# Performance work log

Measured on AMD Instinct MI355X. Metric: run time of the kernel, lower is better.

The kernel has to match this reference:

```python
import jax, jax.numpy as jnp
import numpy as np
import math

B, S, D = 1, 1024, 4096
H, HD, KVH = 32, 128, 8
R, FF = 16, 14336
EPS = 1e-5


def setup_inputs() -> dict:
    key = jax.random.key(0)
    ks = jax.random.split(key, 32)
    def nrm(i, shape, scale):
        return jax.random.normal(ks[i], shape, dtype=jnp.float32) * scale
    inp = {}
    inp["x"] = nrm(0, (B, S, D), 0.5)
    inp["norm_w1"] = jnp.ones((D,), jnp.float32)
    inp["norm_w2"] = jnp.ones((D,), jnp.float32)
    # rotary embedding tables (Mistral theta=10000)
    inv_freq = 1.0 / (10000.0 ** (jnp.arange(0, HD, 2, dtype=jnp.float32) / HD))
    freqs = jnp.outer(jnp.arange(S, dtype=jnp.float32), inv_freq)
    emb = jnp.concatenate([freqs, freqs], axis=-1)  # [S, HD]
    inp["cos"] = jnp.cos(emb)
    inp["sin"] = jnp.sin(emb)
    causal = jnp.tril(jnp.ones((S, S), dtype=bool))
    inp["mask"] = jnp.where(causal, 0.0, -1e9).astype(jnp.float32)[None, None]  # [1,1,S,S]
    w_shapes = {"wq": (D, D), "wk": (KVH * HD, D), "wv": (KVH * HD, D),
                "wo": (D, D), "wg": (FF, D), "wu": (FF, D), "wd": (D, FF)}
    i = 1
    for name, shp in w_shapes.items():
        inp[name] = nrm(i, shp, 0.02); i += 1
        dout, din = shp
        inp["la_" + name[1]] = nrm(i, (din, R), 0.02); i += 1
        inp["lb_" + name[1]] = nrm(i, (R, dout), 0.02); i += 1
    inp["num_heads"] = H
    inp["head_dim"] = HD
    inp["num_kv_heads"] = KVH
    return inp


def _rms(x, w):
    # rmsnorm_forward with eps=1e-5, weight only
    return x * jax.lax.rsqrt(jnp.mean(x * x, axis=-1, keepdims=True) + EPS) * w


def _lora(x, W, la, lb):
    # dequantized base weight [out,in] applied as x @ W.T, plus low-rank delta
    return x @ W.T + (x @ la) @ lb


def _rope(x, cos, sin):
    # x: [B, h, S, HD]; rotate_half convention
    x1, x2 = jnp.split(x, 2, axis=-1)
    rot = jnp.concatenate([-x2, x1], axis=-1)
    return x * cos[None, None] + rot * sin[None, None]


def _layer(x, norm_w1, norm_w2, cos, sin, mask,
           wq, la_q, lb_q, wk, la_k, lb_k, wv, la_v, lb_v, wo, la_o, lb_o,
           wg, la_g, lb_g, wu, la_u, lb_u, wd, la_d, lb_d,
           num_heads, head_dim, num_kv_heads):
    b, s, d = x.shape
    n_rep = num_heads // num_kv_heads
    xn1 = _rms(x, norm_w1)
    q = _lora(xn1, wq, la_q, lb_q).reshape(b, s, num_heads, head_dim).transpose(0, 2, 1, 3)
    k = _lora(xn1, wk, la_k, lb_k).reshape(b, s, num_kv_heads, head_dim).transpose(0, 2, 1, 3)
    v = _lora(xn1, wv, la_v, lb_v).reshape(b, s, num_kv_heads, head_dim).transpose(0, 2, 1, 3)
    q = _rope(q, cos, sin)
    k = _rope(k, cos, sin)
    k = jnp.repeat(k, n_rep, axis=1)
    v = jnp.repeat(v, n_rep, axis=1)
    scores = jnp.einsum("bhqd,bhkd->bhqk", q, k) / math.sqrt(head_dim) + mask
    a = jax.nn.softmax(scores, axis=-1)
    o = jnp.einsum("bhqk,bhkd->bhqd", a, v).transpose(0, 2, 1, 3).reshape(b, s, d)
    o = _lora(o, wo, la_o, lb_o)
    x_med = x + o
    xn2 = _rms(x_med, norm_w2)
    gate = _lora(xn2, wg, la_g, lb_g)
    up = _lora(xn2, wu, la_u, lb_u)
    h = jax.nn.silu(gate) * up
    down = _lora(h, wd, la_d, lb_d)
    return x_med + down


def reference(x, norm_w1, norm_w2, cos, sin, mask,
              wq, la_q, lb_q, wk, la_k, lb_k, wv, la_v, lb_v, wo, la_o, lb_o,
              wg, la_g, lb_g, wu, la_u, lb_u, wd, la_d, lb_d,
              num_heads, head_dim, num_kv_heads):
    return _layer(x, norm_w1, norm_w2, cos, sin, mask,
                  wq, la_q, lb_q, wk, la_k, lb_k, wv, la_v, lb_v, wo, la_o, lb_o,
                  wg, la_g, lb_g, wu, la_u, lb_u, wd, la_d, lb_d,
                  num_heads, head_dim, num_kv_heads)
```

## Files before the change

### kernel.cpp

```cpp
#include <hip/hip_runtime.h>
#include <hip/hip_bf16.h>
#include <math.h>

#define SEQ 1024
#define DIM 4096
#define NH 32
#define HD 128
#define NKVH 8
#define FF 14336
#define LR 16

typedef __attribute__((ext_vector_type(8))) short bf16x8;
typedef __attribute__((ext_vector_type(4))) float f32x4;
typedef __attribute__((ext_vector_type(4))) ushort ushort4v;
typedef __attribute__((ext_vector_type(4))) unsigned int u32x4;

__device__ __forceinline__ ushort f2bf(float f) {
  union { float f; unsigned u; } v; v.f = f;
  unsigned r = (v.u + 0x7FFFu + ((v.u >> 16) & 1u)) >> 16;
  return (ushort)r;
}
__device__ __forceinline__ float bf2f(ushort h) {
  union { unsigned u; float f; } v; v.u = ((unsigned)h) << 16;
  return v.f;
}
__device__ __forceinline__ unsigned cvtpk(float a, float b) {
  unsigned r;
  asm("v_cvt_pk_bf16_f32 %0, %1, %2" : "=v"(r) : "v"(a), "v"(b));
  return r;
}

__device__ __forceinline__ void gload_lds16(const void* g, void* l) {
  __builtin_amdgcn_global_load_lds(
      (const __attribute__((address_space(1))) void*)g,
      (__attribute__((address_space(3))) void*)l, 16, 0, 0);
}

__global__ __launch_bounds__(256) void rmsnorm_kernel(const float* __restrict__ x,
                                                      const float* __restrict__ w,
                                                      ushort* __restrict__ out) {
  int row = blockIdx.x;
  int tid = threadIdx.x;
  const float* xr = x + (size_t)row * DIM;
  float vals[16];
  float s = 0.f;
#pragma unroll
  for (int c = 0; c < 4; c++) {
    float4 v = *(const float4*)&xr[(tid + c * 256) * 4];
    vals[c * 4 + 0] = v.x; vals[c * 4 + 1] = v.y;
    vals[c * 4 + 2] = v.z; vals[c * 4 + 3] = v.w;
    s += v.x * v.x + v.y * v.y + v.z * v.z + v.w * v.w;
  }
#pragma unroll
  for (int off = 32; off >= 1; off >>= 1) s += __shfl_down(s, off);
  __shared__ float wsum[4];
  __shared__ float scale_s;
  int lane = tid & 63, wv = tid >> 6;
  if (lane == 0) wsum[wv] = s;
  __syncthreads();
  if (tid == 0) {
    float t = wsum[0] + wsum[1] + wsum[2] + wsum[3];
    scale_s = rsqrtf(t / (float)DIM + 1e-5f);
  }
  __syncthreads();
  float scale = scale_s;
  ushort* orow = out + (size_t)row * DIM;
#pragma unroll
  for (int c = 0; c < 4; c++) {
    int base = (tid + c * 256) * 4;
    float4 wv4 = *(const float4*)&w[base];
    ushort4v ov;
    ov.x = f2bf(vals[c * 4 + 0] * scale * wv4.x);
    ov.y = f2bf(vals[c * 4 + 1] * scale * wv4.y);
    ov.z = f2bf(vals[c * 4 + 2] * scale * wv4.z);
    ov.w = f2bf(vals[c * 4 + 3] * scale * wv4.w);
    *(ushort4v*)&orow[base] = ov;
  }
}

template <int NL>
__global__ __launch_bounds__(256) void lora_a_kernel(
    const ushort* __restrict__ A,
    const float* __restrict__ la0, const float* __restrict__ la1,
    const float* __restrict__ la2,
    ushort* __restrict__ t0, ushort* __restrict__ t1, ushort* __restrict__ t2,
    int K) {
  int m = blockIdx.x, i = threadIdx.x;
  float acc[NL][16];
#pragma unroll
  for (int l = 0; l < NL; l++)
#pragma unroll
    for (int n = 0; n < 16; n++) acc[l][n] = 0.f;

  const ushort* Arow = A + (size_t)m * K;
  int nc = K >> 8;
  for (int c = 0; c < nc; c++) {
    int k = c * 256 + i;
    float a = bf2f(Arow[k]);
#pragma unroll
    for (int l = 0; l < NL; l++) {
      const float* lap = (l == 0 ? la0 : (l == 1 ? la1 : la2)) + (size_t)k * 16;
#pragma unroll
      for (int q = 0; q < 4; q++) {
        float4 lv = *(const float4*)&lap[q * 4];
        acc[l][q * 4 + 0] += a * lv.x;
        acc[l][q * 4 + 1] += a * lv.y;
        acc[l][q * 4 + 2] += a * lv.z;
        acc[l][q * 4 + 3] += a * lv.w;
      }
    }
  }

  __shared__ float red[256][17];
  __shared__ float red2[16][17];
#pragma unroll
  for (int l = 0; l < NL; l++) {
    __syncthreads();
#pragma unroll
    for (int n = 0; n < 16; n++) red[i][n] = acc[l][n];
    __syncthreads();
    {
      int g = i >> 4, n = i & 15;
      float s = 0.f;
#pragma unroll
      for (int j = 0; j < 16; j++) s += red[g * 16 + j][n];
      red2[g][n] = s;
    }
    __syncthreads();
    if (i < 16) {
      float s2 = 0.f;
#pragma unroll
      for (int g2 = 0; g2 < 16; g2++) s2 += red2[g2][i];
      ushort* tp = (l == 0 ? t0 : (l == 1 ? t1 : t2));
      tp[(size_t)m * LR + i] = f2bf(s2);
    }
  }
}

template <int WM>
__global__ __launch_bounds__(512) void gemm256_kernel(
    const ushort* __restrict__ A,
    const float* __restrict__ W0, const float* __restrict__ W1, const float* __restrict__ W2,
    const float* __restrict__ lb0, const float* __restrict__ lb1, const float* __restrict__ lb2,
    const ushort* __restrict__ t0, const ushort* __restrict__ t1, const ushort* __restrict__ t2,
    void* __restrict__ o0, void* __restrict__ o1, void* __restrict__ o2,
    int c1, int c2, void* __restrict__ outp, int M, int N, int K, int nkp) {
  __shared__ __align__(16) ushort As[2][256 * 64];
  __shared__ __align__(16) ushort Bs[2][256 * 64];
  int tid = threadIdx.x;
  int lane = tid & 63, wave = tid >> 6;
  int wm = wave >> 2, wn = wave & 3;

  int gx = gridDim.x, gy = gridDim.y, gz = gridDim.z;
  int flat = blockIdx.x + gx * (blockIdx.y + gy * blockIdx.z);
  int nwg = gx * gy * gz;
  int q = nwg >> 3, r = nwg & 7;
  int xcd = flat & 7;
  int wgid = (xcd < r ? xcd * (q + 1) : r * (q + 1) + (xcd - r) * q) + (flat >> 3);
  int sh = gy * gz;
  int bx = wgid / sh;
  int rem = wgid - bx * sh;
  int z = rem / gy;
  int by = rem - z * gy;

  int n0 = bx * 256, m0 = by * 256;
  int k0 = z * nkp;

  const float* Wp; const float* lbp; const ushort* tp; void* osel; int nseg, wseg;
  if (n0 < c1)      { Wp = W0; lbp = lb0; tp = t0; osel = o0; nseg = n0;      wseg = c1; }
  else if (n0 < c2) { Wp = W1; lbp = lb1; tp = t1; osel = o1; nseg = n0 - c1; wseg = c2 - c1; }
  else              { Wp = W2; lbp = lb2; tp = t2; osel = o2; nseg = n0 - c2; wseg = N - c2; }

  int srow = tid >> 3;
  int sswz = ((tid & 7) ^ (srow & 7)) * 8;
  const ushort* Ab = A + (size_t)(m0 + srow) * K + sswz;
  const float* Wbase = Wp + (size_t)(nseg + srow) * K + (tid & 7) * 8;

  f32x4 acc[8][4] = {};
  float4 breg[8];

#define SHALF(kt, b, h)                                                       \
  _Pragma("unroll") for (int i = 2 * (h); i < 2 * (h) + 2; i++) {             \
    gload_lds16(Ab + (size_t)(i * 64) * K + (size_t)(kt) * 64,                \
                &As[b][wave * 512 + i * 4096]);                               \
  }
#define BLOAD(kt, h)                                                          \
  {                                                                           \
    const float* gp = Wbase + (size_t)((h) * 128) * K + (size_t)(kt) * 64;    \
    breg[(h) * 4 + 0] = *(const float4*)gp;                                   \
    breg[(h) * 4 + 1] = *(const float4*)(gp + 4);                             \
    breg[(h) * 4 + 2] = *(const float4*)(gp + (size_t)64 * K);                \
    breg[(h) * 4 + 3] = *(const float4*)(gp + (size_t)64 * K + 4);            \
  }
#define WRITE_B(b)                                                            \
  _Pragma("unroll") for (int h = 0; h < 2; h++)                               \
  _Pragma("unroll") for (int j = 0; j < 2; j++) {                             \
    int rr = h * 128 + j * 64 + srow;                                         \
    float4 lo = breg[h * 4 + j * 2 + 0];                                      \
    float4 hi = breg[h * 4 + j * 2 + 1];                                      \
    u32x4 v;                                                                  \
    v.x = cvtpk(lo.x, lo.y); v.y = cvtpk(lo.z, lo.w);                         \
    v.z = cvtpk(hi.x, hi.y); v.w = cvtpk(hi.z, hi.w);                         \
    *(u32x4*)&Bs[b][rr * 64 + (((tid & 7) ^ (rr & 7))) * 8] = v;              \
  }
#define LDFRAG(buf, rr, ks) \
  (*(const bf16x8*)&(buf)[(rr) * 64 + (((ks) * 4 + (lane >> 4)) ^ ((rr) & 7)) * 8])

  BLOAD(k0, 0); BLOAD(k0, 1);
  SHALF(k0, 0, 0); SHALF(k0, 0, 1);
  asm volatile("s_waitcnt vmcnt(4)" ::: "memory");
  WRITE_B(0);
  if (nkp > 1) { BLOAD(k0 + 1, 0); BLOAD(k0 + 1, 1); }
  if (nkp > 1) asm volatile("s_waitcnt vmcnt(8)" ::: "memory");
  else         asm volatile("s_waitcnt vmcnt(0)" ::: "memory");
  asm volatile("s_waitcnt lgkmcnt(0)" ::: "memory");
  __builtin_amdgcn_s_barrier();
  __builtin_amdgcn_sched_barrier(0);

  for (int tau = 0; tau < nkp; tau++) {
    int b = tau & 1;
    bool s1 = (tau + 1 < nkp), s2 = (tau + 2 < nkp);
    const ushort* as = As[b];
    const ushort* bs = Bs[b];
    bf16x8 bfr[4][2];
#pragma unroll
    for (int p = 0; p < 4; p++) {
      bf16x8 af[2][2];
#pragma unroll
      for (int qq = 0; qq < 2; qq++) {
        int ra = wm * 128 + (p * 2 + qq) * 16 + (lane & 15);
#pragma unroll
        for (int ks = 0; ks < 2; ks++) af[qq][ks] = LDFRAG(as, ra, ks);
      }
      if (p == 0) {
#pragma unroll
        for (int f = 0; f < 4; f++) {
          int rb = wn * 64 + f * 16 + (lane & 15);
#pragma unroll
          for (int ks = 0; ks < 2; ks++) bfr[f][ks] = LDFRAG(bs, rb, ks);
        }
      }
      if (p == 0 && s1) { SHALF(k0 + tau + 1, b ^ 1, 0); }
      if (p == 1 && s1) { SHALF(k0 + tau + 1, b ^ 1, 1); }
      if (p == 2 && s2) { BLOAD(k0 + tau + 2, 0); }
      if (p == 3 && s2) { BLOAD(k0 + tau + 2, 1); }
      __builtin_amdgcn_sched_barrier(0);
      __builtin_amdgcn_s_barrier();
      asm volatile("s_waitcnt lgkmcnt(0)" ::: "memory");
      __builtin_amdgcn_sched_barrier(0);
      __builtin_amdgcn_s_setprio(1);
#pragma unroll
      for (int qq = 0; qq < 2; qq++)
#pragma unroll
        for (int fn = 0; fn < 4; fn++)
#pragma unroll
          for (int ks = 0; ks < 2; ks++)
            acc[p * 2 + qq][fn] = __builtin_amdgcn_mfma_f32_16x16x32_bf16(
                af[qq][ks], bfr[fn][ks], acc[p * 2 + qq][fn], 0, 0, 0);
      __builtin_amdgcn_s_setprio(0);
      __builtin_amdgcn_sched_barrier(0);
      if (p == 1 && s1) {
        asm volatile("s_waitcnt vmcnt(4)" ::: "memory");
        WRITE_B(b ^ 1);
        __builtin_amdgcn_sched_barrier(0);
      }
      if (p == 3) {
        if (s2) asm volatile("s_waitcnt vmcnt(8)" ::: "memory");
        else    asm volatile("s_waitcnt vmcnt(0)" ::: "memory");
      }
      __builtin_amdgcn_s_barrier();
      __builtin_amdgcn_sched_barrier(0);
    }
  }
#undef SHALF
#undef BLOAD
#undef WRITE_B

  if (z == 0) {
#pragma unroll
    for (int it = 0; it < 2; it++) {
      int task = tid + it * 512;
      int rr = task >> 2, ls = task & 3;
      int ph = ls ^ (rr & 7);
      bf16x8 avv = {};
      bf16x8 bvv = {};
      if (ls < 2) {
        avv = *(const bf16x8*)&tp[(size_t)(m0 + rr) * LR + ls * 8];
#pragma unroll
        for (int j = 0; j < 8; j++)
          bvv[j] = (short)f2bf(lbp[(size_t)(ls * 8 + j) * wseg + nseg + rr]);
      }
      *(bf16x8*)&As[0][rr * 64 + ph * 8] = avv;
      *(bf16x8*)&Bs[0][rr * 64 + ph * 8] = bvv;
    }
    __syncthreads();
    bf16x8 af[8], bfr[4];
#pragma unroll
    for (int f = 0; f < 8; f++) {
      int ra = wm * 128 + f * 16 + (lane & 15);
      af[f] = LDFRAG(As[0], ra, 0);
    }
#pragma unroll
    for (int f = 0; f < 4; f++) {
      int rb = wn * 64 + f * 16 + (lane & 15);
      bfr[f] = LDFRAG(Bs[0], rb, 0);
    }
#pragma unroll
    for (int fm = 0; fm < 8; fm++)
#pragma unroll
      for (int fn = 0; fn < 4; fn++)
        acc[fm][fn] = __builtin_amdgcn_mfma_f32_16x16x32_bf16(af[fm], bfr[fn], acc[fm][fn], 0, 0, 0);
  }
#undef LDFRAG

#pragma unroll
  for (int fm = 0; fm < 8; fm++) {
#pragma unroll
    for (int j = 0; j < 4; j++) {
      int mg = m0 + wm * 128 + fm * 16 + (lane >> 4) * 4 + j;
#pragma unroll
      for (int fn = 0; fn < 4; fn++) {
        int ncol = wn * 64 + fn * 16 + (lane & 15);
        float v = acc[fm][fn][j];
        if (WM == 0) {
          ((ushort*)osel)[(size_t)mg * wseg + nseg + ncol] = f2bf(v);
        } else {
          ((float*)outp)[((size_t)z * M + mg) * (size_t)N + n0 + ncol] = v;
        }
      }
    }
  }
}

__global__ __launch_bounds__(256) void silu_mul_kernel(const ushort* __restrict__ g,
                                                       const ushort* __restrict__ u,
                                                       ushort* __restrict__ h) {
  size_t idx = (size_t)(blockIdx.x * 256 + threadIdx.x) * 8;
  bf16x8 gv = *(const bf16x8*)&g[idx];
  bf16x8 uv = *(const bf16x8*)&u[idx];
  bf16x8 hv;
#pragma unroll
  for (int i = 0; i < 8; i++) {
    float gf = bf2f((ushort)gv[i]);
    float uf = bf2f((ushort)uv[i]);
    float sv = gf / (1.f + __expf(-gf));
    hv[i] = (short)f2bf(sv * uf);
  }
  *(bf16x8*)&h[idx] = hv;
}

__global__ __launch_bounds__(256) void reduce2_qkv_rope(const float* __restrict__ p,
                                                        const float* __restrict__ ct,
                                                        const float* __restrict__ st,
                                                        ushort* __restrict__ qb,
                                                        ushort* __restrict__ kb,
                                                        ushort* __restrict__ vtb) {
  int gidx = blockIdx.x * 256 + threadIdx.x;
  int r = gidx / 896, j = gidx - r * 896;
  size_t row = (size_t)r * 6144;
  size_t sstride = (size_t)SEQ * 6144;
  if (j < 640) {
    bool isq = j < 512;
    int jj = isq ? j : j - 512;
    int h = jj >> 4, d0 = (jj & 15) * 4;
    size_t base = row + (isq ? 0 : DIM) + h * 128 + d0;
    float4 a1 = *(const float4*)&p[base];
    float4 b1 = *(const float4*)&p[base + sstride];
    float4 a2 = *(const float4*)&p[base + 64];
    float4 b2 = *(const float4*)&p[base + 64 + sstride];
    float4 x1, x2;
    x1.x = a1.x + b1.x; x1.y = a1.y + b1.y; x1.z = a1.z + b1.z; x1.w = a1.w + b1.w;
    x2.x = a2.x + b2.x; x2.y = a2.y + b2.y; x2.z = a2.z + b2.z; x2.w = a2.w + b2.w;
    float4 c = *(const float4*)&ct[r * HD + d0];
    float4 s = *(const float4*)&st[r * HD + d0];
    float sc = isq ? 0.08838834764831845f : 1.0f;
    ushort4v o1, o2;
    o1.x = f2bf((x1.x * c.x - x2.x * s.x) * sc);
    o1.y = f2bf((x1.y * c.y - x2.y * s.y) * sc);
    o1.z = f2bf((x1.z * c.z - x2.z * s.z) * sc);
    o1.w = f2bf((x1.w * c.w - x2.w * s.w) * sc);
    o2.x = f2bf((x2.x * c.x + x1.x * s.x) * sc);
    o2.y = f2bf((x2.y * c.y + x1.y * s.y) * sc);
    o2.z = f2bf((x2.z * c.z + x1.z * s.z) * sc);
    o2.w = f2bf((x2.w * c.w + x1.w * s.w) * sc);
    if (isq) {
      *(ushort4v*)&qb[(size_t)r * DIM + h * 128 + d0] = o1;
      *(ushort4v*)&qb[(size_t)r * DIM + h * 128 + d0 + 64] = o2;
    } else {
      *(ushort4v*)&kb[(size_t)r * 1024 + h * 128 + d0] = o1;
      *(ushort4v*)&kb[(size_t)r * 1024 + h * 128 + d0 + 64] = o2;
    }
  } else {
    int jj = j - 640;
    int c0 = jj * 4;
    size_t base = row + DIM + 1024 + c0;
    float4 a = *(const float4*)&p[base];
    float4 b = *(const float4*)&p[base + sstride];
    vtb[(size_t)(c0 + 0) * SEQ + r] = f2bf(a.x + b.x);
    vtb[(size_t)(c0 + 1) * SEQ + r] = f2bf(a.y + b.y);
    vtb[(size_t)(c0 + 2) * SEQ + r] = f2bf(a.z + b.z);
    vtb[(size_t)(c0 + 3) * SEQ + r] = f2bf(a.w + b.w);
  }
}

__global__ __launch_bounds__(256) void reduce4_res_kernel(const float* __restrict__ p,
                                                          const float* __restrict__ res,
                                                          float* __restrict__ out,
                                                          size_t sstride) {
  size_t i = ((size_t)blockIdx.x * 256 + threadIdx.x) * 4;
  float4 a = *(const float4*)&p[i];
  float4 b = *(const float4*)&p[i + sstride];
  float4 c = *(const float4*)&p[i + 2 * sstride];
  float4 d = *(const float4*)&p[i + 3 * sstride];
  float4 r = *(const float4*)&res[i];
  float4 o;
  o.x = a.x + b.x + c.x + d.x + r.x;
  o.y = a.y + b.y + c.y + d.y + r.y;
  o.z = a.z + b.z + c.z + d.z + r.z;
  o.w = a.w + b.w + c.w + d.w + r.w;
  *(float4*)&out[i] = o;
}

__global__ __launch_bounds__(256) void reduce4_res_rms(const float* __restrict__ p,
                                                       const float* __restrict__ res,
                                                       const float* __restrict__ w,
                                                       float* __restrict__ xmed,
                                                       ushort* __restrict__ xn2,
                                                       size_t sstride) {
  int row = blockIdx.x, tid = threadIdx.x;
  size_t base = (size_t)row * DIM;
  float vals[16];
  float sq = 0.f;
#pragma unroll
  for (int c = 0; c < 4; c++) {
    size_t i = base + (tid + c * 256) * 4;
    float4 a = *(const float4*)&p[i];
    float4 b = *(const float4*)&p[i + sstride];
    float4 cc = *(const float4*)&p[i + 2 * sstride];
    float4 d = *(const float4*)&p[i + 3 * sstride];
    float4 r = *(const float4*)&res[i];
    float4 v;
    v.x = a.x + b.x + cc.x + d.x + r.x;
    v.y = a.y + b.y + cc.y + d.y + r.y;
    v.z = a.z + b.z + cc.z + d.z + r.z;
    v.w = a.w + b.w + cc.w + d.w + r.w;
    *(float4*)&xmed[i] = v;
    vals[c * 4 + 0] = v.x; vals[c * 4 + 1] = v.y;
    vals[c * 4 + 2] = v.z; vals[c * 4 + 3] = v.w;
    sq += v.x * v.x + v.y * v.y + v.z * v.z + v.w * v.w;
  }
#pragma unroll
  for (int off = 32; off >= 1; off >>= 1) sq += __shfl_down(sq, off);
  __shared__ float wsum[4];
  __shared__ float scale_s;
  int lane = tid & 63, wv = tid >> 6;
  if (lane == 0) wsum[wv] = sq;
  __syncthreads();
  if (tid == 0) {
    float t = wsum[0] + wsum[1] + wsum[2] + wsum[3];
    scale_s = rsqrtf(t / (float)DIM + 1e-5f);
  }
  __syncthreads();
  float scale = scale_s;
#pragma unroll
  for (int c = 0; c < 4; c++) {
    int off = (tid + c * 256) * 4;
    float4 wv4 = *(const float4*)&w[off];
    ushort4v ov;
    ov.x = f2bf(vals[c * 4 + 0] * scale * wv4.x);
    ov.y = f2bf(vals[c * 4 + 1] * scale * wv4.y);
    ov.z = f2bf(vals[c * 4 + 2] * scale * wv4.z);
    ov.w = f2bf(vals[c * 4 + 3] * scale * wv4.w);
    *(ushort4v*)&xn2[base + off] = ov;
  }
}

__global__ __launch_bounds__(256) void attn_kernel(const ushort* __restrict__ q,
                                                   const ushort* __restrict__ k,
                                                   const ushort* __restrict__ vt,
                                                   ushort* __restrict__ o) {
  int flat = blockIdx.x + 16 * blockIdx.y;
  int kvh = flat & 7;
  int idx = flat >> 3;
  int h = kvh * 4 + (idx & 3);
  int qb = 15 - (idx >> 2);
  int tid = threadIdx.x, lane = tid & 63, wave = tid >> 6;
  __shared__ ushort Ks[64][136];
  __shared__ ushort Vs[128][72];
  __shared__ ushort Ps[4][16][72];

  bf16x8 qf[4];
  int qrow = qb * 64 + wave * 16 + (lane & 15);
#pragma unroll
  for (int kk = 0; kk < 4; kk++)
    qf[kk] = *(const bf16x8*)&q[(size_t)qrow * DIM + h * HD + kk * 32 + (lane >> 4) * 8];

  f32x4 oacc[8] = {};
  float mrow[4], lrow[4];
  int qr[4];
#pragma unroll
  for (int j = 0; j < 4; j++) {
    mrow[j] = -INFINITY; lrow[j] = 0.f;
    qr[j] = qb * 64 + wave * 16 + (lane >> 4) * 4 + j;
  }

  for (int kt = 0; kt <= qb; kt++) {
    int key0 = kt * 64;
#pragma unroll
    for (int c = 0; c < 4; c++) {
      int e = tid * 32 + c * 8;
      int r = e >> 7, cc = e & 127;
      *(bf16x8*)&Ks[r][cc] =
          *(const bf16x8*)&k[(size_t)(key0 + r) * (NKVH * HD) + kvh * HD + cc];
      int r2 = e >> 6, cc2 = e & 63;
      *(bf16x8*)&Vs[r2][cc2] =
          *(const bf16x8*)&vt[(size_t)(kvh * HD + r2) * SEQ + key0 + cc2];
    }
    __syncthreads();

    f32x4 sf[4] = {};
#pragma unroll
    for (int fn = 0; fn < 4; fn++)
#pragma unroll
      for (int kk = 0; kk < 4; kk++) {
        bf16x8 kf = *(const bf16x8*)&Ks[fn * 16 + (lane & 15)][kk * 32 + (lane >> 4) * 8];
        sf[fn] = __builtin_amdgcn_mfma_f32_16x16x32_bf16(qf[kk], kf, sf[fn], 0, 0, 0);
      }

#pragma unroll
    for (int fn = 0; fn < 4; fn++) {
      int key = key0 + fn * 16 + (lane & 15);
#pragma unroll
      for (int j = 0; j < 4; j++)
        if (key > qr[j]) sf[fn][j] = -INFINITY;
    }

#pragma unroll
    for (int j = 0; j < 4; j++) {
      float mx = fmaxf(fmaxf(sf[0][j], sf[1][j]), fmaxf(sf[2][j], sf[3][j]));
#pragma unroll
      for (int off = 1; off < 16; off <<= 1) mx = fmaxf(mx, __shfl_xor(mx, off));
      float mnew = fmaxf(mrow[j], mx);
      float sc = __expf(mrow[j] - mnew);
      mrow[j] = mnew;
      float rs = 0.f;
#pragma unroll
      for (int fn = 0; fn < 4; fn++) {
        float p = __expf(sf[fn][j] - mnew);
        sf[fn][j] = p;
        rs += p;
      }
#pragma unroll
      for (int off = 1; off < 16; off <<= 1) rs += __shfl_xor(rs, off);
      lrow[j] = lrow[j] * sc + rs;
#pragma unroll
      for (int f2 = 0; f2 < 8; f2++) oacc[f2][j] *= sc;
    }

#pragma unroll
    for (int fn = 0; fn < 4; fn++)
#pragma unroll
      for (int j = 0; j < 4; j++)
        Ps[wave][(lane >> 4) * 4 + j][fn * 16 + (lane & 15)] = f2bf(sf[fn][j]);

#pragma unroll
    for (int kk = 0; kk < 2; kk++) {
      bf16x8 pf = *(const bf16x8*)&Ps[wave][lane & 15][kk * 32 + (lane >> 4) * 8];
#pragma unroll
      for (int f2 = 0; f2 < 8; f2++) {
        bf16x8 vf = *(const bf16x8*)&Vs[f2 * 16 + (lane & 15)][kk * 32 + (lane >> 4) * 8];
        oacc[f2] = __builtin_amdgcn_mfma_f32_16x16x32_bf16(pf, vf, oacc[f2], 0, 0, 0);
      }
    }
    __syncthreads();
  }

#pragma unroll
  for (int j = 0; j < 4; j++) {
    float inv = 1.f / lrow[j];
#pragma unroll
    for (int f2 = 0; f2 < 8; f2++)
      o[(size_t)qr[j] * DIM + h * HD + f2 * 16 + (lane & 15)] = f2bf(oacc[f2][j] * inv);
  }
}

extern "C" void kernel_launch(void* const* d_in, const int* in_sizes, int n_in,
                              void* d_out, int out_size, void* d_ws, size_t ws_size,
                              hipStream_t stream) {
  const float* x    = (const float*)d_in[0];
  const float* w1   = (const float*)d_in[1];
  const float* w2   = (const float*)d_in[2];
  const float* cosT = (const float*)d_in[3];
  const float* sinT = (const float*)d_in[4];
  const float* wq = (const float*)d_in[6];
  const float* la_q = (const float*)d_in[7];
  const float* lb_q = (const float*)d_in[8];
  const float* wk = (const float*)d_in[9];
  const float* la_k = (const float*)d_in[10];
  const float* lb_k = (const float*)d_in[11];
  const float* wv = (const float*)d_in[12];
  const float* la_v = (const float*)d_in[13];
  const float* lb_v = (const float*)d_in[14];
  const float* wo = (const float*)d_in[15];
  const float* la_o = (const float*)d_in[16];
  const float* lb_o = (const float*)d_in[17];
  const float* wg = (const float*)d_in[18];
  const float* la_g = (const float*)d_in[19];
  const float* lb_g = (const float*)d_in[20];
  const float* wu = (const float*)d_in[21];
  const float* la_u = (const float*)d_in[22];
  const float* lb_u = (const float*)d_in[23];
  const float* wd = (const float*)d_in[24];
  const float* la_d = (const float*)d_in[25];
  const float* lb_d = (const float*)d_in[26];
  float* out = (float*)d_out;

  char* ws = (char*)d_ws;
  ushort* xn1 = (ushort*)ws;  ws += (size_t)SEQ * DIM * 2;
  ushort* qb  = (ushort*)ws;  ws += (size_t)SEQ * DIM * 2;
  ushort* kb  = (ushort*)ws;  ws += (size_t)SEQ * NKVH * HD * 2;
  ushort* vtb = (ushort*)ws;  ws += (size_t)SEQ * NKVH * HD * 2;
  ushort* ob  = (ushort*)ws;  ws += (size_t)SEQ * DIM * 2;
  float*  xmed= (float*)ws;   ws += (size_t)SEQ * DIM * 4;
  ushort* xn2 = (ushort*)ws;  ws += (size_t)SEQ * DIM * 2;
  ushort* gate= (ushort*)ws;  ws += (size_t)SEQ * FF * 2;
  ushort* up  = (ushort*)ws;  ws += (size_t)SEQ * FF * 2;
  ushort* hb  = (ushort*)ws;  ws += (size_t)SEQ * FF * 2;
  ushort* t_q = (ushort*)ws; ws += SEQ * LR * 2;
  ushort* t_k = (ushort*)ws; ws += SEQ * LR * 2;
  ushort* t_v = (ushort*)ws; ws += SEQ * LR * 2;
  ushort* t_o = (ushort*)ws; ws += SEQ * LR * 2;
  ushort* t_g = (ushort*)ws; ws += SEQ * LR * 2;
  ushort* t_u = (ushort*)ws; ws += SEQ * LR * 2;
  ushort* t_d = (ushort*)ws; ws += SEQ * LR * 2;

  float* pbuf1 = (float*)gate;
  float* pbuf2 = (float*)xn2;

  size_t snd = (size_t)SEQ * DIM;

  rmsnorm_kernel<<<SEQ, 256, 0, stream>>>(x, w1, xn1);
  lora_a_kernel<3><<<SEQ, 256, 0, stream>>>(xn1, la_q, la_k, la_v, t_q, t_k, t_v, DIM);

  gemm256_kernel<3><<<dim3((DIM + 2048) / 256, SEQ / 256, 2), 512, 0, stream>>>(
      xn1, wq, wk, wv, lb_q, lb_k, lb_v, t_q, t_k, t_v,
      nullptr, nullptr, nullptr, DIM, DIM + 1024,
      pbuf1, SEQ, DIM + 2048, DIM, 32);
  reduce2_qkv_rope<<<SEQ * 896 / 256, 256, 0, stream>>>(pbuf1, cosT, sinT, qb, kb, vtb);

  attn_kernel<<<dim3(SEQ / 64, NH), 256, 0, stream>>>(qb, kb, vtb, ob);

  lora_a_kernel<1><<<SEQ, 256, 0, stream>>>(ob, la_o, la_o, la_o, t_o, t_o, t_o, DIM);
  gemm256_kernel<3><<<dim3(DIM / 256, SEQ / 256, 4), 512, 0, stream>>>(
      ob, wo, wo, wo, lb_o, lb_o, lb_o, t_o, t_o, t_o,
      nullptr, nullptr, nullptr, DIM, DIM,
      pbuf1, SEQ, DIM, DIM, 16);
  reduce4_res_rms<<<SEQ, 256, 0, stream>>>(pbuf1, x, w2, xmed, xn2, snd);

  lora_a_kernel<2><<<SEQ, 256, 0, stream>>>(xn2, la_g, la_u, la_u, t_g, t_u, t_u, DIM);
  gemm256_kernel<0><<<dim3(2 * FF / 256, SEQ / 256, 1), 512, 0, stream>>>(
      xn2, wg, wu, wu, lb_g, lb_u, lb_u, t_g, t_u, t_u,
      gate, up, up, FF, 2 * FF,
      nullptr, SEQ, 2 * FF, DIM, DIM / 64);
  silu_mul_kernel<<<SEQ * FF / 8 / 256, 256, 0, stream>>>(gate, up, hb);
  lora_a_kernel<1><<<SEQ, 256, 0, stream>>>(hb, la_d, la_d, la_d, t_d, t_d, t_d, FF);
  gemm256_kernel<3><<<dim3(DIM / 256, SEQ / 256, 4), 512, 0, stream>>>(
      hb, wd, wd, wd, lb_d, lb_d, lb_d, t_d, t_d, t_d,
      nullptr, nullptr, nullptr, DIM, DIM,
      pbuf2, SEQ, DIM, FF, FF / 4 / 64);
  reduce4_res_kernel<<<snd / 1024, 256, 0, stream>>>(pbuf2, xmed, out, snd);
}
```

Before: 873.3 us.

## Store split-K partials in bf16 and raise QKV split-K to four

The split-K GEMM partial outputs are now written as bf16 instead of fp32, which halves the partial-buffer write and read traffic for the reduction kernels. The QKV projection also moves from a 2-way to a 4-way K split (16 k-tiles each), giving 384 workgroups instead of 192 for better CU occupancy. The reduce kernels now sum four bf16 partials. This adds rounding error on every partial before accumulation, and the QKV reduction reads more slices.

```diff
diff --git a/kernel.cpp b/kernel.cpp
--- a/kernel.cpp
+++ b/kernel.cpp
@@ -27,6 +27,15 @@
 __device__ __forceinline__ unsigned cvtpk(float a, float b) {
   unsigned r;
   asm("v_cvt_pk_bf16_f32 %0, %1, %2" : "=v"(r) : "v"(a), "v"(b));
+  return r;
+}
+__device__ __forceinline__ float4 sum4v(const ushort* __restrict__ p, size_t idx, size_t ss) {
+  float4 r = {0.f, 0.f, 0.f, 0.f};
+#pragma unroll
+  for (int s = 0; s < 4; s++) {
+    ushort4v v = *(const ushort4v*)&p[idx + (size_t)s * ss];
+    r.x += bf2f(v.x); r.y += bf2f(v.y); r.z += bf2f(v.z); r.w += bf2f(v.w);
+  }
   return r;
 }
 
@@ -325,7 +334,7 @@
         if (WM == 0) {
           ((ushort*)osel)[(size_t)mg * wseg + nseg + ncol] = f2bf(v);
         } else {
-          ((float*)outp)[((size_t)z * M + mg) * (size_t)N + n0 + ncol] = v;
+          ((ushort*)outp)[((size_t)z * M + mg) * (size_t)N + n0 + ncol] = f2bf(v);
         }
       }
     }
@@ -349,7 +358,7 @@
   *(bf16x8*)&h[idx] = hv;
 }
 
-__global__ __launch_bounds__(256) void reduce2_qkv_rope(const float* __restrict__ p,
+__global__ __launch_bounds__(256) void reduce4_qkv_rope(const ushort* __restrict__ p,
                                                         const float* __restrict__ ct,
                                                         const float* __restrict__ st,
                                                         ushort* __restrict__ qb,
@@ -358,19 +367,14 @@
   int gidx = blockIdx.x * 256 + threadIdx.x;
   int r = gidx / 896, j = gidx - r * 896;
   size_t row = (size_t)r * 6144;
-  size_t sstride = (size_t)SEQ * 6144;
+  size_t ss = (size_t)SEQ * 6144;
   if (j < 640) {
     bool isq = j < 512;
     int jj = isq ? j : j - 512;
     int h = jj >> 4, d0 = (jj & 15) * 4;
     size_t base = row + (isq ? 0 : DIM) + h * 128 + d0;
-    float4 a1 = *(const float4*)&p[base];
-    float4 b1 = *(const float4*)&p[base + sstride];
-    float4 a2 = *(const float4*)&p[base + 64];
-    float4 b2 = *(const float4*)&p[base + 64 + sstride];
-    float4 x1, x2;
-    x1.x = a1.x + b1.x; x1.y = a1.y + b1.y; x1.z = a1.z + b1.z; x1.w = a1.w + b1.w;
-    x2.x = a2.x + b2.x; x2.y = a2.y + b2.y; x2.z = a2.z + b2.z; x2.w = a2.w + b2.w;
+    float4 x1 = sum4v(p, base, ss);
+    float4 x2 = sum4v(p, base + 64, ss);
     float4 c = *(const float4*)&ct[r * HD + d0];
     float4 s = *(const float4*)&st[r * HD + d0];
     float sc = isq ? 0.08838834764831845f : 1.0f;
@@ -394,34 +398,27 @@
     int jj = j - 640;
     int c0 = jj * 4;
     size_t base = row + DIM + 1024 + c0;
-    float4 a = *(const float4*)&p[base];
-    float4 b = *(const float4*)&p[base + sstride];
-    vtb[(size_t)(c0 + 0) * SEQ + r] = f2bf(a.x + b.x);
-    vtb[(size_t)(c0 + 1) * SEQ + r] = f2bf(a.y + b.y);
-    vtb[(size_t)(c0 + 2) * SEQ + r] = f2bf(a.z + b.z);
-    vtb[(size_t)(c0 + 3) * SEQ + r] = f2bf(a.w + b.w);
-  }
-}
-
-__global__ __launch_bounds__(256) void reduce4_res_kernel(const float* __restrict__ p,
+    float4 sv = sum4v(p, base, ss);
+    vtb[(size_t)(c0 + 0) * SEQ + r] = f2bf(sv.x);
+    vtb[(size_t)(c0 + 1) * SEQ + r] = f2bf(sv.y);
+    vtb[(size_t)(c0 + 2) * SEQ + r] = f2bf(sv.z);
+    vtb[(size_t)(c0 + 3) * SEQ + r] = f2bf(sv.w);
+  }
+}
+
+__global__ __launch_bounds__(256) void reduce4_res_kernel(const ushort* __restrict__ p,
                                                           const float* __restrict__ res,
                                                           float* __restrict__ out,
                                                           size_t sstride) {
   size_t i = ((size_t)blockIdx.x * 256 + threadIdx.x) * 4;
-  float4 a = *(const float4*)&p[i];
-  float4 b = *(const float4*)&p[i + sstride];
-  float4 c = *(const float4*)&p[i + 2 * sstride];
-  float4 d = *(const float4*)&p[i + 3 * sstride];
+  float4 sv = sum4v(p, i, sstride);
   float4 r = *(const float4*)&res[i];
   float4 o;
-  o.x = a.x + b.x + c.x + d.x + r.x;
-  o.y = a.y + b.y + c.y + d.y + r.y;
-  o.z = a.z + b.z + c.z + d.z + r.z;
-  o.w = a.w + b.w + c.w + d.w + r.w;
+  o.x = sv.x + r.x; o.y = sv.y + r.y; o.z = sv.z + r.z; o.w = sv.w + r.w;
   *(float4*)&out[i] = o;
 }
 
-__global__ __launch_bounds__(256) void reduce4_res_rms(const float* __restrict__ p,
+__global__ __launch_bounds__(256) void reduce4_res_rms(const ushort* __restrict__ p,
                                                        const float* __restrict__ res,
                                                        const float* __restrict__ w,
                                                        float* __restrict__ xmed,
@@ -434,16 +431,10 @@
 #pragma unroll
   for (int c = 0; c < 4; c++) {
     size_t i = base + (tid + c * 256) * 4;
-    float4 a = *(const float4*)&p[i];
-    float4 b = *(const float4*)&p[i + sstride];
-    float4 cc = *(const float4*)&p[i + 2 * sstride];
-    float4 d = *(const float4*)&p[i + 3 * sstride];
+    float4 sv = sum4v(p, i, sstride);
     float4 r = *(const float4*)&res[i];
     float4 v;
-    v.x = a.x + b.x + cc.x + d.x + r.x;
-    v.y = a.y + b.y + cc.y + d.y + r.y;
-    v.z = a.z + b.z + cc.z + d.z + r.z;
-    v.w = a.w + b.w + cc.w + d.w + r.w;
+    v.x = sv.x + r.x; v.y = sv.y + r.y; v.z = sv.z + r.z; v.w = sv.w + r.w;
     *(float4*)&xmed[i] = v;
     vals[c * 4 + 0] = v.x; vals[c * 4 + 1] = v.y;
     vals[c * 4 + 2] = v.z; vals[c * 4 + 3] = v.w;
@@ -634,19 +625,19 @@
   ushort* t_u = (ushort*)ws; ws += SEQ * LR * 2;
   ushort* t_d = (ushort*)ws; ws += SEQ * LR * 2;
 
-  float* pbuf1 = (float*)gate;
-  float* pbuf2 = (float*)xn2;
+  ushort* pbuf1 = (ushort*)gate;
+  ushort* pbuf2 = (ushort*)xn2;
 
   size_t snd = (size_t)SEQ * DIM;
 
   rmsnorm_kernel<<<SEQ, 256, 0, stream>>>(x, w1, xn1);
   lora_a_kernel<3><<<SEQ, 256, 0, stream>>>(xn1, la_q, la_k, la_v, t_q, t_k, t_v, DIM);
 
-  gemm256_kernel<3><<<dim3((DIM + 2048) / 256, SEQ / 256, 2), 512, 0, stream>>>(
+  gemm256_kernel<3><<<dim3((DIM + 2048) / 256, SEQ / 256, 4), 512, 0, stream>>>(
       xn1, wq, wk, wv, lb_q, lb_k, lb_v, t_q, t_k, t_v,
       nullptr, nullptr, nullptr, DIM, DIM + 1024,
-      pbuf1, SEQ, DIM + 2048, DIM, 32);
-  reduce2_qkv_rope<<<SEQ * 896 / 256, 256, 0, stream>>>(pbuf1, cosT, sinT, qb, kb, vtb);
+      pbuf1, SEQ, DIM + 2048, DIM, 16);
+  reduce4_qkv_rope<<<SEQ * 896 / 256, 256, 0, stream>>>(pbuf1, cosT, sinT, qb, kb, vtb);
 
   attn_kernel<<<dim3(SEQ / 64, NH), 256, 0, stream>>>(qb, kb, vtb, ob);
 
```

Result: no change. 863.5 us (-1.1%).
